# Kernel optimization log

Hardware: AMD Instinct MI355X
Metric: run time of the kernel (lower is better)

Reference implementation:

```python
import jax, jax.numpy as jnp
import numpy as np
import math

N_NODES = 100000
N_EDGES = 1600000
INPUT_SIZE = 256
N_HEADS = 8
HEAD_SIZE = INPUT_SIZE // N_HEADS  # 32
DK = math.sqrt(HEAD_SIZE)


def setup_inputs() -> dict:
    key = jax.random.key(0)
    k1, k2, k3, k4, k5 = jax.random.split(key, 5)
    X = jax.random.normal(k1, (N_NODES, INPUT_SIZE), dtype=jnp.float32)
    edge_index = jax.random.randint(k2, (2, N_EDGES), 0, N_NODES, dtype=jnp.int64)
    # kaiming_normal (fan_in = input_size) std = sqrt(2/fan_in)
    std = math.sqrt(2.0 / INPUT_SIZE)
    Wq = jax.random.normal(k3, (INPUT_SIZE, HEAD_SIZE), dtype=jnp.float32) * std
    Wk = jax.random.normal(k4, (INPUT_SIZE, HEAD_SIZE), dtype=jnp.float32) * std
    Wv = jax.random.normal(k5, (INPUT_SIZE, HEAD_SIZE), dtype=jnp.float32) * std
    return {"X": X, "edge_index": edge_index, "Wq": Wq, "Wk": Wk, "Wv": Wv}


def reference(X, edge_index, Wq, Wk, Wv):
    N = X.shape[0]
    Q = X @ Wq  # [N, h]
    K = X @ Wk  # [N, h]
    V = X @ Wv  # [N, h]
    src = edge_index[0]  # row index (softmax over dim=1 -> per-src segments)
    dst = edge_index[1]
    # per-edge QK dot, scaled
    scores = jnp.sum(Q[src] * K[dst], axis=-1) / DK  # [E]
    # segment-wise (sparse) softmax over each row
    row_max = jax.ops.segment_max(scores, src, num_segments=N)  # [N]
    ex = jnp.exp(scores - row_max[src])  # [E]
    denom = jax.ops.segment_sum(ex, src, num_segments=N)  # [N]
    alpha = ex / denom[src]  # [E]
    # sparse-mm aggregate of V: out[i] = sum_j alpha_ij * V[j]
    out = jax.ops.segment_sum(alpha[:, None] * V[dst], src, num_segments=N)  # [N, h]
    return out
```

## Files before the change

kernel.cpp:

```cpp
#include <hip/hip_runtime.h>

#define N_INPUT 256
#define HS 32

#define BKT_SHIFT 7
#define BKT_NODES 128
#define NBUCK_MAX 800
#define CAP 2560
#define EPB 2048

typedef __attribute__((ext_vector_type(8))) short bf16x8;
typedef __attribute__((ext_vector_type(4))) float f32x4;
typedef __attribute__((ext_vector_type(8))) unsigned short u16x8;

__device__ __forceinline__ unsigned short f2bf(float f) {
    unsigned u = __float_as_uint(f);
    unsigned r = u + 0x7FFFu + ((u >> 16) & 1u);
    return (unsigned short)(r >> 16);
}
__device__ __forceinline__ float bf2f(unsigned short u) {
    return __uint_as_float((unsigned)u << 16);
}

__global__ void prep_kernel(int* __restrict__ gtail, int nb,
                            const float* __restrict__ Wq,
                            const float* __restrict__ Wk,
                            const float* __restrict__ Wv,
                            uint4* __restrict__ Wp) {
    int t = threadIdx.x;
    if (blockIdx.x == 0) {
        for (int i = t; i < nb; i += 256) gtail[i] = 0;
        return;
    }
    int c = (int)(blockIdx.x - 1) * 256 + t;
    int s = c >> 9;
    int tt = (c >> 6) & 7;
    int L = c & 63;
    const float* wm = (s < 2) ? Wq : (s < 4) ? Wk : Wv;
    const float* wsrc = wm + (size_t)(tt * 32 + (L >> 4) * 8) * HS + (s & 1) * 16 + (L & 15);
    unsigned e0 = f2bf(wsrc[0 * HS]) | ((unsigned)f2bf(wsrc[1 * HS]) << 16);
    unsigned e1 = f2bf(wsrc[2 * HS]) | ((unsigned)f2bf(wsrc[3 * HS]) << 16);
    unsigned e2 = f2bf(wsrc[4 * HS]) | ((unsigned)f2bf(wsrc[5 * HS]) << 16);
    unsigned e3 = f2bf(wsrc[6 * HS]) | ((unsigned)f2bf(wsrc[7 * HS]) << 16);
    Wp[c] = make_uint4(e0, e1, e2, e3);
}

__global__ __launch_bounds__(256) void mega_kernel(
        const float* __restrict__ X, const uint4* __restrict__ Wp,
        const int* __restrict__ src, const int* __restrict__ dst,
        float* __restrict__ Q, unsigned short* __restrict__ KVb,
        int* __restrict__ gtail, unsigned* __restrict__ staging,
        int N, int E, int nb, int s1blocks) {
    __shared__ int sh[NBUCK_MAX];
    __shared__ int sbs[NBUCK_MAX];
    int tid = threadIdx.x;
    int idx = (int)blockIdx.x;
    bool is_s1 = (idx % 3 == 0) && (idx / 3 < s1blocks);

    if (is_s1) {
        int e0 = (idx / 3) * EPB;
        for (int i = tid; i < nb; i += 256) sh[i] = 0;
        __syncthreads();
        int ss[8], dd[8], rr[8];
#pragma unroll
        for (int k = 0; k < 8; ++k) {
            int i = e0 + tid + k * 256;
            ss[k] = -1;
            if (i < E) {
                int s = src[i];
                dd[k] = dst[i];
                ss[k] = s;
                rr[k] = atomicAdd(&sh[s >> BKT_SHIFT], 1);
            }
        }
        __syncthreads();
        for (int b = tid; b < nb; b += 256) {
            int c = sh[b];
            sbs[b] = c ? atomicAdd(&gtail[b], c) : 0;
        }
        __syncthreads();
#pragma unroll
        for (int k = 0; k < 8; ++k) {
            if (ss[k] >= 0) {
                int b = ss[k] >> BKT_SHIFT;
                int pos = sbs[b] + rr[k];
                if (pos < CAP)
                    staging[(size_t)b * CAP + pos] =
                        ((unsigned)(ss[k] & (BKT_NODES - 1)) << 17) | (unsigned)dd[k];
            }
        }
        return;
    }

    int bq = idx - min(idx / 3 + 1, s1blocks);
    int wave = tid >> 6;
    int L = tid & 63;
    int quad = L >> 4;
    int lane16 = L & 15;
    int mt = bq * 4 + wave;
    if (mt * 16 >= N) return;

    const float* xrow = X + (size_t)(mt * 16 + lane16) * N_INPUT + quad * 8;
    bf16x8 afrag[8];
#pragma unroll
    for (int t = 0; t < 8; ++t) {
        float4 a0 = *(const float4*)(xrow + t * 32);
        float4 a1 = *(const float4*)(xrow + t * 32 + 4);
        bf16x8 f;
        f[0] = (short)f2bf(a0.x); f[1] = (short)f2bf(a0.y);
        f[2] = (short)f2bf(a0.z); f[3] = (short)f2bf(a0.w);
        f[4] = (short)f2bf(a1.x); f[5] = (short)f2bf(a1.y);
        f[6] = (short)f2bf(a1.z); f[7] = (short)f2bf(a1.w);
        afrag[t] = f;
    }

#pragma unroll
    for (int s = 0; s < 6; ++s) {
        f32x4 acc = {0.f, 0.f, 0.f, 0.f};
#pragma unroll
        for (int t = 0; t < 8; ++t) {
            bf16x8 bfrag = ((const bf16x8*)Wp)[(s * 8 + t) * 64 + L];
            acc = __builtin_amdgcn_mfma_f32_16x16x32_bf16(afrag[t], bfrag, acc, 0, 0, 0);
        }
        int col = (s & 1) * 16 + lane16;
#pragma unroll
        for (int r = 0; r < 4; ++r) {
            int row = mt * 16 + quad * 4 + r;
            if (s < 2) {
                Q[(size_t)row * HS + col] = acc[r];
            } else {
                size_t pos = (size_t)row * 64 + (size_t)(col >> 2) * 8 +
                             ((s < 4) ? 0 : 4) + (col & 3);
                KVb[pos] = f2bf(acc[r]);
            }
        }
    }
}

__global__ __launch_bounds__(512) void s2_agg_kernel(
        const unsigned* __restrict__ staging, const int* __restrict__ gtail,
        const float* __restrict__ Q, const unsigned short* __restrict__ KVb,
        float* __restrict__ out, int N) {
    __shared__ int ldst[CAP];
    __shared__ int nh[BKT_NODES];
    __shared__ int nx[BKT_NODES];
    __shared__ int rk[BKT_NODES];
    int b = blockIdx.x;
    int t = threadIdx.x;
    int cnt = min(gtail[b], CAP);
    if (t < BKT_NODES) { nh[t] = 0; rk[t] = 0; }
    __syncthreads();
    unsigned stash[5];
#pragma unroll
    for (int k = 0; k < 5; ++k) {
        int i = t + k * 512;
        if (i < cnt) {
            unsigned e = staging[(size_t)b * CAP + i];
            stash[k] = e;
            atomicAdd(&nh[e >> 17], 1);
        }
    }
    __syncthreads();
    if (t < BKT_NODES) nx[t] = nh[t];
    __syncthreads();
    for (int off = 1; off < BKT_NODES; off <<= 1) {
        int u = (t >= off && t < BKT_NODES) ? nx[t - off] : 0;
        __syncthreads();
        if (t < BKT_NODES) nx[t] += u;
        __syncthreads();
    }
#pragma unroll
    for (int k = 0; k < 5; ++k) {
        int i = t + k * 512;
        if (i < cnt) {
            unsigned e = stash[k];
            int sl = (int)(e >> 17);
            int r = atomicAdd(&rk[sl], 1);
            ldst[nx[sl] - nh[sl] + r] = (int)(e & 0x1FFFFu);
        }
    }
    __syncthreads();

    int lane = t & 31;
    int grp = t >> 5;
    int slot = lane >> 3;
    int sub = lane & 7;
    int node0 = b << BKT_SHIFT;
    for (int ni = grp; ni < BKT_NODES; ni += 16) {
        int n = node0 + ni;
        if (n >= N) continue;
        int end = nx[ni];
        int beg = end - nh[ni];
        float4 qf = *(const float4*)(Q + (size_t)n * HS + sub * 4);
        float4 acc = make_float4(0.f, 0.f, 0.f, 0.f);
        float den = 0.f;
        int d0 = (beg + slot < end) ? ldst[beg + slot] : 0;
        u16x8 kvc = *(const u16x8*)(KVb + (size_t)d0 * 64 + sub * 8);
        for (int j = beg; j < end; j += 4) {
            bool valid = (j + slot) < end;
            u16x8 kv = kvc;
            int jn = j + 4;
            if (jn < end) {
                int dn = (jn + slot < end) ? ldst[jn + slot] : 0;
                kvc = *(const u16x8*)(KVb + (size_t)dn * 64 + sub * 8);
            }
            float p = qf.x * bf2f(kv[0]) + qf.y * bf2f(kv[1]) +
                      qf.z * bf2f(kv[2]) + qf.w * bf2f(kv[3]);
            p += __shfl_xor(p, 1, 32);
            p += __shfl_xor(p, 2, 32);
            p += __shfl_xor(p, 4, 32);
            float ex = valid ? __expf(p * 0.17677669529663687f) : 0.f;
            den += ex;
            acc.x += ex * bf2f(kv[4]);
            acc.y += ex * bf2f(kv[5]);
            acc.z += ex * bf2f(kv[6]);
            acc.w += ex * bf2f(kv[7]);
        }
#pragma unroll
        for (int off = 8; off <= 16; off <<= 1) {
            acc.x += __shfl_xor(acc.x, off, 32);
            acc.y += __shfl_xor(acc.y, off, 32);
            acc.z += __shfl_xor(acc.z, off, 32);
            acc.w += __shfl_xor(acc.w, off, 32);
            den += __shfl_xor(den, off, 32);
        }
        if (lane < 8) {
            float4 o = make_float4(0.f, 0.f, 0.f, 0.f);
            if (end > beg) {
                float rd = 1.f / den;
                o = make_float4(acc.x * rd, acc.y * rd, acc.z * rd, acc.w * rd);
            }
            *(float4*)(out + (size_t)n * HS + lane * 4) = o;
        }
    }
}

extern "C" void kernel_launch(void* const* d_in, const int* in_sizes, int n_in,
                              void* d_out, int out_size, void* d_ws, size_t ws_size,
                              hipStream_t stream) {
    const float* X  = (const float*)d_in[0];
    const int*   ei = (const int*)d_in[1];
    const float* Wq = (const float*)d_in[2];
    const float* Wk = (const float*)d_in[3];
    const float* Wv = (const float*)d_in[4];

    int N = in_sizes[0] / N_INPUT;
    int E = in_sizes[1] / 2;
    const int* src = ei;
    const int* dst = ei + E;

    float* ws = (float*)d_ws;
    float* Q = ws;
    unsigned short* KVb = (unsigned short*)(Q + (size_t)N * HS);
    uint4* Wp = (uint4*)(KVb + (size_t)N * 64);
    int* gtail = (int*)(Wp + 3072);
    unsigned* staging = (unsigned*)(gtail + NBUCK_MAX);
    float* out = (float*)d_out;

    int nbuck = (N + BKT_NODES - 1) >> BKT_SHIFT;
    int s1blocks = (E + EPB - 1) / EPB;
    int mtiles = (N + 15) / 16;
    int qblocks = (mtiles + 3) / 4;

    prep_kernel<<<13, 256, 0, stream>>>(gtail, nbuck, Wq, Wk, Wv, Wp);
    mega_kernel<<<s1blocks + qblocks, 256, 0, stream>>>(
        X, Wp, src, dst, Q, KVb, gtail, staging, N, E, nbuck, s1blocks);
    s2_agg_kernel<<<nbuck, 512, 0, stream>>>(staging, gtail, Q, KVb, out, N);
}
```

Measured before the change: 229.3 us.

## Replicate bucket tail counters to cut global atomic contention in edge binning

Each bucket's global tail counter and staging region is split into 8 replicas selected by edge-block index, so edge-binning blocks contend on different atomics and write to separate sub-regions. The aggregation kernel now reads the replicas in sequence and re-reads staging from global memory instead of stashing entries in registers. The X loads in the projection also switch to nontemporal loads. The per-replica capacity of 416 is only about 2x the expected count, which risks silently dropping edges if buckets are skewed, and staging grows in size.

```diff
diff --git a/kernel.cpp b/kernel.cpp
--- a/kernel.cpp
+++ b/kernel.cpp
@@ -7,6 +7,8 @@
 #define BKT_NODES 128
 #define NBUCK_MAX 800
 #define CAP 2560
+#define NREP 8
+#define CAPR 416
 #define EPB 2048
 
 typedef __attribute__((ext_vector_type(8))) short bf16x8;
@@ -29,7 +31,7 @@
                             uint4* __restrict__ Wp) {
     int t = threadIdx.x;
     if (blockIdx.x == 0) {
-        for (int i = t; i < nb; i += 256) gtail[i] = 0;
+        for (int i = t; i < NREP * NBUCK_MAX; i += 256) gtail[i] = 0;
         return;
     }
     int c = (int)(blockIdx.x - 1) * 256 + t;
@@ -58,7 +60,9 @@
     bool is_s1 = (idx % 3 == 0) && (idx / 3 < s1blocks);
 
     if (is_s1) {
-        int e0 = (idx / 3) * EPB;
+        int sb = idx / 3;
+        int rep = sb & (NREP - 1);
+        int e0 = sb * EPB;
         for (int i = tid; i < nb; i += 256) sh[i] = 0;
         __syncthreads();
         int ss[8], dd[8], rr[8];
@@ -76,7 +80,7 @@
         __syncthreads();
         for (int b = tid; b < nb; b += 256) {
             int c = sh[b];
-            sbs[b] = c ? atomicAdd(&gtail[b], c) : 0;
+            sbs[b] = c ? atomicAdd(&gtail[rep * NBUCK_MAX + b], c) : 0;
         }
         __syncthreads();
 #pragma unroll
@@ -84,8 +88,8 @@
             if (ss[k] >= 0) {
                 int b = ss[k] >> BKT_SHIFT;
                 int pos = sbs[b] + rr[k];
-                if (pos < CAP)
-                    staging[(size_t)b * CAP + pos] =
+                if (pos < CAPR)
+                    staging[((size_t)b * NREP + rep) * CAPR + pos] =
                         ((unsigned)(ss[k] & (BKT_NODES - 1)) << 17) | (unsigned)dd[k];
             }
         }
@@ -104,13 +108,13 @@
     bf16x8 afrag[8];
 #pragma unroll
     for (int t = 0; t < 8; ++t) {
-        float4 a0 = *(const float4*)(xrow + t * 32);
-        float4 a1 = *(const float4*)(xrow + t * 32 + 4);
+        f32x4 a0 = __builtin_nontemporal_load((const f32x4*)(xrow + t * 32));
+        f32x4 a1 = __builtin_nontemporal_load((const f32x4*)(xrow + t * 32 + 4));
         bf16x8 f;
-        f[0] = (short)f2bf(a0.x); f[1] = (short)f2bf(a0.y);
-        f[2] = (short)f2bf(a0.z); f[3] = (short)f2bf(a0.w);
-        f[4] = (short)f2bf(a1.x); f[5] = (short)f2bf(a1.y);
-        f[6] = (short)f2bf(a1.z); f[7] = (short)f2bf(a1.w);
+        f[0] = (short)f2bf(a0[0]); f[1] = (short)f2bf(a0[1]);
+        f[2] = (short)f2bf(a0[2]); f[3] = (short)f2bf(a0[3]);
+        f[4] = (short)f2bf(a1[0]); f[5] = (short)f2bf(a1[1]);
+        f[6] = (short)f2bf(a1[2]); f[7] = (short)f2bf(a1[3]);
         afrag[t] = f;
     }
 
@@ -147,18 +151,22 @@
     __shared__ int rk[BKT_NODES];
     int b = blockIdx.x;
     int t = threadIdx.x;
-    int cnt = min(gtail[b], CAP);
+    int cnt_r[NREP];
+    int total = 0;
+#pragma unroll
+    for (int r = 0; r < NREP; ++r) {
+        int c = min(gtail[r * NBUCK_MAX + b], CAPR);
+        c = min(c, CAP - total);
+        cnt_r[r] = c;
+        total += c;
+    }
     if (t < BKT_NODES) { nh[t] = 0; rk[t] = 0; }
     __syncthreads();
-    unsigned stash[5];
-#pragma unroll
-    for (int k = 0; k < 5; ++k) {
-        int i = t + k * 512;
-        if (i < cnt) {
-            unsigned e = staging[(size_t)b * CAP + i];
-            stash[k] = e;
-            atomicAdd(&nh[e >> 17], 1);
-        }
+#pragma unroll
+    for (int r = 0; r < NREP; ++r) {
+        const unsigned* sg = staging + ((size_t)b * NREP + r) * CAPR;
+        for (int i = t; i < cnt_r[r]; i += 512)
+            atomicAdd(&nh[sg[i] >> 17], 1);
     }
     __syncthreads();
     if (t < BKT_NODES) nx[t] = nh[t];
@@ -170,13 +178,13 @@
         __syncthreads();
     }
 #pragma unroll
-    for (int k = 0; k < 5; ++k) {
-        int i = t + k * 512;
-        if (i < cnt) {
-            unsigned e = stash[k];
+    for (int r = 0; r < NREP; ++r) {
+        const unsigned* sg = staging + ((size_t)b * NREP + r) * CAPR;
+        for (int i = t; i < cnt_r[r]; i += 512) {
+            unsigned e = sg[i];
             int sl = (int)(e >> 17);
-            int r = atomicAdd(&rk[sl], 1);
-            ldst[nx[sl] - nh[sl] + r] = (int)(e & 0x1FFFFu);
+            int rr = atomicAdd(&rk[sl], 1);
+            ldst[nx[sl] - nh[sl] + rr] = (int)(e & 0x1FFFFu);
         }
     }
     __syncthreads();
@@ -254,7 +262,7 @@
     unsigned short* KVb = (unsigned short*)(Q + (size_t)N * HS);
     uint4* Wp = (uint4*)(KVb + (size_t)N * 64);
     int* gtail = (int*)(Wp + 3072);
-    unsigned* staging = (unsigned*)(gtail + NBUCK_MAX);
+    unsigned* staging = (unsigned*)(gtail + NREP * NBUCK_MAX);
     float* out = (float*)d_out;
 
     int nbuck = (N + BKT_NODES - 1) >> BKT_SHIFT;
```

Result: no change. 228.1 us (-0.5%).
